# Performance work log

Measured on AMD Instinct MI355X. Metric: run time of the kernel, lower is better.

The kernel has to match this reference:

```python
import jax, jax.numpy as jnp
import numpy as np
from math import sqrt

FACTOR = 5


def setup_inputs() -> dict:
    key = jax.random.key(0)
    k1, k2, k3, k4 = jax.random.split(key, 4)
    B, L, H, E = 2, 2048, 8, 64
    sample_k = FACTOR * int(np.ceil(np.log(L)))  # 40
    return {
        "queries": jax.random.normal(k1, (B, L, H, E), dtype=jnp.float32),
        "keys": jax.random.normal(k2, (B, L, H, E), dtype=jnp.float32),
        "values": jax.random.normal(k3, (B, L, H, E), dtype=jnp.float32),
        "index_sample": jax.random.randint(k4, (L, sample_k), 0, L, dtype=jnp.int64),
    }


def reference(queries, keys, values, index_sample):
    B, L_Q, H, E = queries.shape
    L_K = keys.shape[1]
    # n_top queries to keep (u in the torch code)
    u = min(FACTOR * int(np.ceil(np.log(L_Q))), L_Q)

    Q = jnp.transpose(queries, (0, 2, 1, 3))  # [B,H,L_Q,E]
    K = jnp.transpose(keys, (0, 2, 1, 3))     # [B,H,L_K,E]
    V = jnp.transpose(values, (0, 2, 1, 3))   # [B,H,L_V,E]

    # --- _prob_QK: sampled scores -> sparsity measure M -> top-u queries ---
    # K_sample[b,h,l,s,:] = K[b,h,index_sample[l,s],:]  -> [B,H,L_Q,S,E]
    K_sample = K[:, :, index_sample, :]
    Q_K_sample = jnp.einsum('bhle,bhlse->bhls', Q, K_sample)  # [B,H,L_Q,S]
    M = Q_K_sample.max(axis=-1) - Q_K_sample.sum(axis=-1) / L_K  # [B,H,L_Q]
    _, M_top = jax.lax.top_k(M, u)  # [B,H,u]

    Q_reduce = jnp.take_along_axis(Q, M_top[..., None], axis=2)  # [B,H,u,E]
    scores = jnp.einsum('bhue,bhke->bhuk', Q_reduce, K)          # [B,H,u,L_K]

    # --- scale (scale=None -> 1/sqrt(E)) ---
    scores = scores * (1.0 / sqrt(E))

    # --- initial context: mean of V broadcast over queries ---
    context = jnp.broadcast_to(V.mean(axis=2, keepdims=True), (B, H, L_Q, E))

    # --- update context at selected query rows ---
    attn = jax.nn.softmax(scores, axis=-1)          # [B,H,u,L_K]
    ctx_upd = jnp.einsum('bhuk,bhke->bhue', attn, V)  # [B,H,u,E]
    bI = jnp.arange(B)[:, None, None]
    hI = jnp.arange(H)[None, :, None]
    context = context.at[bI, hI, M_top].set(ctx_upd)

    attns = jnp.full((B, H, L_K, L_K), 1.0 / L_K, dtype=attn.dtype)
    attns = attns.at[bI, hI, M_top].set(attn)

    return jnp.transpose(context, (0, 2, 1, 3)), attns
```

## Files before the change

kernel.cpp:

```cpp
#include <hip/hip_runtime.h>

#define B_  2
#define L_  2048
#define H_  8
#define E_  64
#define U_  40
#define LK_ 2048

#define KA_BLOCKS 8192

typedef float floatv4 __attribute__((ext_vector_type(4)));

__global__ __launch_bounds__(256) void kAVm(
    const float* __restrict__ Q, const float* __restrict__ K,
    const float* __restrict__ V, const int* __restrict__ idxs,
    float* __restrict__ M, float* __restrict__ partialV, int S) {
  if (blockIdx.x < KA_BLOCKS) {
    int wave = blockIdx.x * 4 + (threadIdx.x >> 6);
    int lane = threadIdx.x & 63;
    int l = wave & (L_ - 1);
    int h = (wave >> 11) & (H_ - 1);
    int b = wave >> 14;
    int g = lane >> 4;
    int e4 = lane & 15;
    const float4* Q4 = (const float4*)Q;
    const float4* K4 = (const float4*)K;
    int qrow = ((b * L_ + l) * H_ + h) << 4;
    float4 qv = Q4[qrow + e4];
    int myidx = (lane < S) ? idxs[(size_t)l * S + lane] : 0;
    float vmax = -3.0e38f, vsum = 0.0f;
    int nb = (S + 3) >> 2;
#pragma unroll 2
    for (int t = 0; t < nb; ++t) {
      int s = 4 * t + g;
      int kidx = __shfl(myidx, (s < S) ? s : 0, 64);
      int krow = ((b * L_ + kidx) * H_ + h) << 4;
      float4 kv = K4[krow + e4];
      float p = qv.x * kv.x + qv.y * kv.y + qv.z * kv.z + qv.w * kv.w;
      p += __shfl_xor(p, 1, 64);
      p += __shfl_xor(p, 2, 64);
      p += __shfl_xor(p, 4, 64);
      p += __shfl_xor(p, 8, 64);
      if (s < S) { vmax = fmaxf(vmax, p); vsum += p; }
    }
    vmax = fmaxf(vmax, __shfl_xor(vmax, 16, 64));
    vmax = fmaxf(vmax, __shfl_xor(vmax, 32, 64));
    vsum += __shfl_xor(vsum, 16, 64);
    vsum += __shfl_xor(vsum, 32, 64);
    if (lane == 0) M[(b * H_ + h) * L_ + l] = vmax - vsum * (1.0f / (float)LK_);
  } else {
    int blk = blockIdx.x - KA_BLOCKS;
    int bh = blk >> 3, c = blk & 7;
    int b = bh >> 3, h = bh & 7;
    int t = threadIdx.x, lane = t & 63, w = t >> 6;
    int l0 = c * 256 + w * 64;
    float acc = 0.0f;
#pragma unroll 4
    for (int i = 0; i < 64; ++i)
      acc += V[(((b * L_ + l0 + i) * H_ + h) << 6) + lane];
    __shared__ float cred[4][64];
    cred[w][lane] = acc;
    __syncthreads();
    if (w == 0)
      partialV[(bh * 8 + c) * 64 + lane] =
          cred[0][lane] + cred[1][lane] + cred[2][lane] + cred[3][lane];
  }
}

__global__ __launch_bounds__(64) void kB2_topk(
    const float* __restrict__ M, const float* __restrict__ partialV,
    int* __restrict__ Mtop, float* __restrict__ meanV) {
  int bh = blockIdx.x;
  int lane = threadIdx.x;
  float v[32];
  int base = bh * L_;
#pragma unroll
  for (int i = 0; i < 32; ++i) v[i] = M[base + lane + i * 64];
  for (int it = 0; it < U_; ++it) {
    float best = -3.0e38f;
    int bi = 0x7fffffff;
#pragma unroll
    for (int i = 0; i < 32; ++i) {
      if (v[i] > best) { best = v[i]; bi = lane + i * 64; }
    }
#pragma unroll
    for (int off = 32; off > 0; off >>= 1) {
      float ov = __shfl_xor(best, off, 64);
      int oi = __shfl_xor(bi, off, 64);
      if (ov > best || (ov == best && oi < bi)) { best = ov; bi = oi; }
    }
    if (lane == 0) Mtop[bh * U_ + it] = bi;
    if ((bi & 63) == lane) {
#pragma unroll
      for (int i = 0; i < 32; ++i)
        if ((bi >> 6) == i) v[i] = -3.0e38f;
    }
  }
  float s = 0.0f;
#pragma unroll
  for (int c = 0; c < 8; ++c) s += partialV[(bh * 8 + c) * 64 + lane];
  meanV[(bh << 6) + lane] = s * (1.0f / (float)L_);
}

__global__ __launch_bounds__(256) void kC_fill(
    floatv4* __restrict__ out0, floatv4* __restrict__ out1,
    const float* __restrict__ meanV) {
  const int N0 = (B_ * L_ * H_ * E_) / 4;
  const int N1 = (B_ * H_ * LK_ * LK_) / 4;
  const float iv = 1.0f / (float)LK_;
  const floatv4 fv = {iv, iv, iv, iv};
  int stride = gridDim.x * blockDim.x;
  int tid = blockIdx.x * blockDim.x + threadIdx.x;
  for (int i = tid; i < N0; i += stride) {
    int e4 = i & 15;
    int h = (i >> 4) & 7;
    int b = i >> 18;
    const floatv4* mp = (const floatv4*)(meanV + ((((b << 3) + h)) << 6));
    __builtin_nontemporal_store(mp[e4], &out0[i]);
  }
  for (int i = tid; i < N1; i += stride) {
    __builtin_nontemporal_store(fv, &out1[i]);
  }
}

__global__ __launch_bounds__(256) void kD_scores(
    const float* __restrict__ Q, const float* __restrict__ K,
    const int* __restrict__ Mtop, float* __restrict__ out1) {
  int bh = blockIdx.x >> 5;
  int kc = blockIdx.x & 31;
  int b = bh >> 3, h = bh & 7;
  __shared__ float Kt[64][65];
  __shared__ float Qt[U_][65];
  __shared__ int rows[U_];
  int t = threadIdx.x;
  int k0 = kc << 6;
  for (int i = t; i < 64 * 64; i += 256) {
    int r = i >> 6, e = i & 63;
    Kt[r][e] = K[(((b * L_ + k0 + r) * H_ + h) << 6) + e];
  }
  if (t < U_) rows[t] = Mtop[bh * U_ + t];
  __syncthreads();
  for (int i = t; i < U_ * 64; i += 256) {
    int u = i >> 6, e = i & 63;
    Qt[u][e] = Q[(((b * L_ + rows[u]) * H_ + h) << 6) + e];
  }
  __syncthreads();
  for (int p = t; p < U_ * 64; p += 256) {
    int u = p >> 6, k = p & 63;
    float s = 0.0f;
#pragma unroll
    for (int e = 0; e < 64; ++e) s += Qt[u][e] * Kt[k][e];
    out1[(size_t)(bh * LK_ + rows[u]) * LK_ + (k0 + k)] = s * 0.125f;
  }
}

__global__ __launch_bounds__(256) void kE_softmax_ctx(
    const float* __restrict__ V, const int* __restrict__ Mtop,
    float* __restrict__ out0, float* __restrict__ out1) {
  int gblk = blockIdx.x;
  int u = gblk % U_;
  int bh = gblk / U_;
  int b = bh >> 3, h = bh & 7;
  int t = threadIdx.x, lane = t & 63, w = t >> 6;
  int lu = Mtop[bh * U_ + u];
  float* row = out1 + (size_t)(bh * LK_ + lu) * LK_;
  float4* row4 = (float4*)row;
  float4 v0 = row4[t], v1 = row4[t + 256];
  float lmax = fmaxf(fmaxf(fmaxf(v0.x, v0.y), fmaxf(v0.z, v0.w)),
                     fmaxf(fmaxf(v1.x, v1.y), fmaxf(v1.z, v1.w)));
#pragma unroll
  for (int off = 32; off > 0; off >>= 1) lmax = fmaxf(lmax, __shfl_xor(lmax, off, 64));
  __shared__ float sred[4];
  if (lane == 0) sred[w] = lmax;
  __syncthreads();
  float gmax = fmaxf(fmaxf(sred[0], sred[1]), fmaxf(sred[2], sred[3]));
  __syncthreads();
  v0.x = __expf(v0.x - gmax); v0.y = __expf(v0.y - gmax);
  v0.z = __expf(v0.z - gmax); v0.w = __expf(v0.w - gmax);
  v1.x = __expf(v1.x - gmax); v1.y = __expf(v1.y - gmax);
  v1.z = __expf(v1.z - gmax); v1.w = __expf(v1.w - gmax);
  float lsum = v0.x + v0.y + v0.z + v0.w + v1.x + v1.y + v1.z + v1.w;
#pragma unroll
  for (int off = 32; off > 0; off >>= 1) lsum += __shfl_xor(lsum, off, 64);
  if (lane == 0) sred[w] = lsum;
  __syncthreads();
  float gsum = sred[0] + sred[1] + sred[2] + sred[3];
  float inv = 1.0f / gsum;
  v0.x *= inv; v0.y *= inv; v0.z *= inv; v0.w *= inv;
  v1.x *= inv; v1.y *= inv; v1.z *= inv; v1.w *= inv;
  __shared__ __attribute__((aligned(16))) float ps[2048];
  float4* ps4 = (float4*)ps;
  ps4[t] = v0; ps4[t + 256] = v1;
  row4[t] = v0; row4[t + 256] = v1;
  __syncthreads();
  int g = lane >> 4, e4 = lane & 15;
  const float4* V4 = (const float4*)V;
  float4 acc = make_float4(0.f, 0.f, 0.f, 0.f);
  int kbase = w << 9;
#pragma unroll 4
  for (int kk = 0; kk < 512; kk += 4) {
    int k = kbase + kk + g;
    float pk = ps[k];
    int vrow = ((b * L_ + k) * H_ + h) << 4;
    float4 vv = V4[vrow + e4];
    acc.x += pk * vv.x; acc.y += pk * vv.y;
    acc.z += pk * vv.z; acc.w += pk * vv.w;
  }
#pragma unroll
  for (int off = 16; off <= 32; off <<= 1) {
    acc.x += __shfl_xor(acc.x, off, 64);
    acc.y += __shfl_xor(acc.y, off, 64);
    acc.z += __shfl_xor(acc.z, off, 64);
    acc.w += __shfl_xor(acc.w, off, 64);
  }
  __shared__ __attribute__((aligned(16))) float credf[4][64];
  if (lane < 16) *(float4*)&credf[w][e4 * 4] = acc;
  __syncthreads();
  if (w == 0) {
    float c = credf[0][lane] + credf[1][lane] + credf[2][lane] + credf[3][lane];
    out0[(((b * L_ + lu) * H_ + h) << 6) + lane] = c;
  }
}

extern "C" void kernel_launch(void* const* d_in, const int* in_sizes, int n_in,
                              void* d_out, int out_size, void* d_ws, size_t ws_size,
                              hipStream_t stream) {
  const float* Q = (const float*)d_in[0];
  const float* K = (const float*)d_in[1];
  const float* V = (const float*)d_in[2];
  const int* idxs = (const int*)d_in[3];
  int S = in_sizes[3] / L_;

  float* out0 = (float*)d_out;
  float* out1 = out0 + (size_t)B_ * L_ * H_ * E_;

  float* M = (float*)d_ws;
  int* Mtop = (int*)((char*)d_ws + (size_t)32768 * 4);
  float* meanV = (float*)((char*)d_ws + (size_t)(32768 + 640) * 4);
  float* partialV = (float*)((char*)d_ws + (size_t)(32768 + 640 + 1024) * 4);

  kAVm<<<dim3(KA_BLOCKS + B_ * H_ * 8), dim3(256), 0, stream>>>(Q, K, V, idxs, M, partialV, S);
  kB2_topk<<<dim3(B_ * H_), dim3(64), 0, stream>>>(M, partialV, Mtop, meanV);
  kC_fill<<<dim3(4096), dim3(256), 0, stream>>>((floatv4*)out0, (floatv4*)out1, meanV);
  kD_scores<<<dim3(B_ * H_ * 32), dim3(256), 0, stream>>>(Q, K, Mtop, out1);
  kE_softmax_ctx<<<dim3(B_ * H_ * U_), dim3(256), 0, stream>>>(V, Mtop, out0, out1);
}
```

Measured before the change: 421.1 us.

## Fuse attns fill into sampling kernel and context fill into scores kernel

Removes the separate fill kernel. Every third block of the first kernel now writes the constant 1/L_K attention fill, so the large store stream overlaps the gather-heavy M computation. The mean-V broadcast into the context output moves into the scores kernel. This saves a launch and lets the bandwidth-bound fill share time with latency-bound work. The risk is that the fill is not ordered before the score writes in kD; the kernel boundaries still keep that ordering.

Result: faster. 401.0 us (-4.8%).

```diff
diff --git a/kernel.cpp b/kernel.cpp
--- a/kernel.cpp
+++ b/kernel.cpp
@@ -7,49 +7,59 @@
 #define U_  40
 #define LK_ 2048
 
-#define KA_BLOCKS 8192
-
 typedef float floatv4 __attribute__((ext_vector_type(4)));
 
-__global__ __launch_bounds__(256) void kAVm(
+__global__ __launch_bounds__(256) void kAF(
     const float* __restrict__ Q, const float* __restrict__ K,
     const float* __restrict__ V, const int* __restrict__ idxs,
-    float* __restrict__ M, float* __restrict__ partialV, int S) {
-  if (blockIdx.x < KA_BLOCKS) {
-    int wave = blockIdx.x * 4 + (threadIdx.x >> 6);
-    int lane = threadIdx.x & 63;
-    int l = wave & (L_ - 1);
-    int h = (wave >> 11) & (H_ - 1);
-    int b = wave >> 14;
-    int g = lane >> 4;
-    int e4 = lane & 15;
-    const float4* Q4 = (const float4*)Q;
-    const float4* K4 = (const float4*)K;
-    int qrow = ((b * L_ + l) * H_ + h) << 4;
-    float4 qv = Q4[qrow + e4];
-    int myidx = (lane < S) ? idxs[(size_t)l * S + lane] : 0;
-    float vmax = -3.0e38f, vsum = 0.0f;
-    int nb = (S + 3) >> 2;
+    float* __restrict__ M, float* __restrict__ partialV,
+    floatv4* __restrict__ out1v, int S) {
+  int bx = blockIdx.x;
+  if (bx < 12288) {
+    int grp = bx / 3, r = bx - grp * 3;
+    if (r < 2) {
+      int wave = (grp * 2 + r) * 4 + (threadIdx.x >> 6);
+      int lane = threadIdx.x & 63;
+      int l = wave & (L_ - 1);
+      int h = (wave >> 11) & (H_ - 1);
+      int b = wave >> 14;
+      int g = lane >> 4;
+      int e4 = lane & 15;
+      const float4* Q4 = (const float4*)Q;
+      const float4* K4 = (const float4*)K;
+      int qrow = ((b * L_ + l) * H_ + h) << 4;
+      float4 qv = Q4[qrow + e4];
+      int myidx = (lane < S) ? idxs[(size_t)l * S + lane] : 0;
+      float vmax = -3.0e38f, vsum = 0.0f;
+      int nb = (S + 3) >> 2;
 #pragma unroll 2
-    for (int t = 0; t < nb; ++t) {
-      int s = 4 * t + g;
-      int kidx = __shfl(myidx, (s < S) ? s : 0, 64);
-      int krow = ((b * L_ + kidx) * H_ + h) << 4;
-      float4 kv = K4[krow + e4];
-      float p = qv.x * kv.x + qv.y * kv.y + qv.z * kv.z + qv.w * kv.w;
-      p += __shfl_xor(p, 1, 64);
-      p += __shfl_xor(p, 2, 64);
-      p += __shfl_xor(p, 4, 64);
-      p += __shfl_xor(p, 8, 64);
-      if (s < S) { vmax = fmaxf(vmax, p); vsum += p; }
-    }
-    vmax = fmaxf(vmax, __shfl_xor(vmax, 16, 64));
-    vmax = fmaxf(vmax, __shfl_xor(vmax, 32, 64));
-    vsum += __shfl_xor(vsum, 16, 64);
-    vsum += __shfl_xor(vsum, 32, 64);
-    if (lane == 0) M[(b * H_ + h) * L_ + l] = vmax - vsum * (1.0f / (float)LK_);
+      for (int t = 0; t < nb; ++t) {
+        int s = 4 * t + g;
+        int kidx = __shfl(myidx, (s < S) ? s : 0, 64);
+        int krow = ((b * L_ + kidx) * H_ + h) << 4;
+        float4 kv = K4[krow + e4];
+        float p = qv.x * kv.x + qv.y * kv.y + qv.z * kv.z + qv.w * kv.w;
+        p += __shfl_xor(p, 1, 64);
+        p += __shfl_xor(p, 2, 64);
+        p += __shfl_xor(p, 4, 64);
+        p += __shfl_xor(p, 8, 64);
+        if (s < S) { vmax = fmaxf(vmax, p); vsum += p; }
+      }
+      vmax = fmaxf(vmax, __shfl_xor(vmax, 16, 64));
+      vmax = fmaxf(vmax, __shfl_xor(vmax, 32, 64));
+      vsum += __shfl_xor(vsum, 16, 64);
+      vsum += __shfl_xor(vsum, 32, 64);
+      if (lane == 0) M[(b * H_ + h) * L_ + l] = vmax - vsum * (1.0f / (float)LK_);
+    } else {
+      const float iv = 1.0f / (float)LK_;
+      const floatv4 fv = {iv, iv, iv, iv};
+      int base = grp * 4096 + threadIdx.x;
+#pragma unroll
+      for (int j = 0; j < 16; ++j)
+        __builtin_nontemporal_store(fv, &out1v[base + j * 256]);
+    }
   } else {
-    int blk = blockIdx.x - KA_BLOCKS;
+    int blk = bx - 12288;
     int bh = blk >> 3, c = blk & 7;
     int b = bh >> 3, h = bh & 7;
     int t = threadIdx.x, lane = t & 63, w = t >> 6;
@@ -102,30 +112,10 @@
   meanV[(bh << 6) + lane] = s * (1.0f / (float)L_);
 }
 
-__global__ __launch_bounds__(256) void kC_fill(
-    floatv4* __restrict__ out0, floatv4* __restrict__ out1,
-    const float* __restrict__ meanV) {
-  const int N0 = (B_ * L_ * H_ * E_) / 4;
-  const int N1 = (B_ * H_ * LK_ * LK_) / 4;
-  const float iv = 1.0f / (float)LK_;
-  const floatv4 fv = {iv, iv, iv, iv};
-  int stride = gridDim.x * blockDim.x;
-  int tid = blockIdx.x * blockDim.x + threadIdx.x;
-  for (int i = tid; i < N0; i += stride) {
-    int e4 = i & 15;
-    int h = (i >> 4) & 7;
-    int b = i >> 18;
-    const floatv4* mp = (const floatv4*)(meanV + ((((b << 3) + h)) << 6));
-    __builtin_nontemporal_store(mp[e4], &out0[i]);
-  }
-  for (int i = tid; i < N1; i += stride) {
-    __builtin_nontemporal_store(fv, &out1[i]);
-  }
-}
-
 __global__ __launch_bounds__(256) void kD_scores(
     const float* __restrict__ Q, const float* __restrict__ K,
-    const int* __restrict__ Mtop, float* __restrict__ out1) {
+    const int* __restrict__ Mtop, float* __restrict__ out1,
+    floatv4* __restrict__ out0v, const float* __restrict__ meanV) {
   int bh = blockIdx.x >> 5;
   int kc = blockIdx.x & 31;
   int b = bh >> 3, h = bh & 7;
@@ -151,6 +141,19 @@
 #pragma unroll
     for (int e = 0; e < 64; ++e) s += Qt[u][e] * Kt[k][e];
     out1[(size_t)(bh * LK_ + rows[u]) * LK_ + (k0 + k)] = s * 0.125f;
+  }
+  const int N0 = (B_ * L_ * H_ * E_) / 4;
+  int gtid = blockIdx.x * 256 + t;
+#pragma unroll
+  for (int j = 0; j < 4; ++j) {
+    int i = gtid + j * 512 * 256;
+    if (i < N0) {
+      int e4 = i & 15;
+      int hh = (i >> 4) & 7;
+      int bb = i >> 18;
+      const floatv4* mp = (const floatv4*)(meanV + (((bb << 3) + hh) << 6));
+      __builtin_nontemporal_store(mp[e4], &out0v[i]);
+    }
   }
 }
 
@@ -239,9 +242,10 @@
   float* meanV = (float*)((char*)d_ws + (size_t)(32768 + 640) * 4);
   float* partialV = (float*)((char*)d_ws + (size_t)(32768 + 640 + 1024) * 4);
 
-  kAVm<<<dim3(KA_BLOCKS + B_ * H_ * 8), dim3(256), 0, stream>>>(Q, K, V, idxs, M, partialV, S);
+  kAF<<<dim3(12288 + B_ * H_ * 8), dim3(256), 0, stream>>>(
+      Q, K, V, idxs, M, partialV, (floatv4*)out1, S);
   kB2_topk<<<dim3(B_ * H_), dim3(64), 0, stream>>>(M, partialV, Mtop, meanV);
-  kC_fill<<<dim3(4096), dim3(256), 0, stream>>>((floatv4*)out0, (floatv4*)out1, meanV);
-  kD_scores<<<dim3(B_ * H_ * 32), dim3(256), 0, stream>>>(Q, K, Mtop, out1);
+  kD_scores<<<dim3(B_ * H_ * 32), dim3(256), 0, stream>>>(
+      Q, K, Mtop, out1, (floatv4*)out0, meanV);
   kE_softmax_ctx<<<dim3(B_ * H_ * U_), dim3(256), 0, stream>>>(V, Mtop, out0, out1);
 }
```
